# Optimization experiments

Hardware: AMD Instinct MI355X
Metric: run time of the kernel (lower is better)

The kernel has to match this reference:

```python
import jax, jax.numpy as jnp
import numpy as np

NUM_HEADS = 12

def setup_inputs() -> dict:
    key = jax.random.key(0)
    ks = jax.random.split(key, 6)
    B, N, C = 8, 1024, 768
    x = jax.random.normal(ks[0], (B, N, C), dtype=jnp.float32)
    qkv_w = jax.random.normal(ks[1], (3 * C, C), dtype=jnp.float32) * 0.02
    qkv_b = jax.random.normal(ks[2], (3 * C,), dtype=jnp.float32) * 0.02
    static_a = jax.random.normal(ks[3], (1, NUM_HEADS, N, N), dtype=jnp.float32) * 0.02
    proj_w = jax.random.normal(ks[4], (C, C), dtype=jnp.float32) * 0.02
    proj_b = jax.random.normal(ks[5], (C,), dtype=jnp.float32) * 0.02
    return {"x": x, "qkv_w": qkv_w, "qkv_b": qkv_b, "static_a": static_a,
            "proj_w": proj_w, "proj_b": proj_b}

def reference(x, qkv_w, qkv_b, static_a, proj_w, proj_b):
    B, N, C = x.shape
    H = NUM_HEADS
    D = C // H
    scale = D ** -0.5
    # qkv: [B,N,3C] -> [3,B,H,N,D]
    qkv = (x @ qkv_w.T + qkv_b).reshape(B, N, 3, H, D).transpose(2, 0, 3, 1, 4)
    q, k, v = qkv[0], qkv[1], qkv[2]
    attn = jnp.einsum('bhnd,bhmd->bhnm', q, k) * scale
    attn = jax.nn.softmax(attn, axis=-1)
    attn = attn + static_a  # static bias added AFTER softmax (no renorm)
    out = jnp.einsum('bhnm,bhmd->bhnd', attn, v)  # [B,H,N,D]
    out = out.transpose(0, 2, 1, 3).reshape(B, N, C)
    return out @ proj_w.T + proj_b
```

## Files before the change

kernel.cpp:

```cpp
#include <hip/hip_runtime.h>
#include <math.h>

#define NB   8
#define SEQ  1024
#define CH   768
#define NH   12
#define HD   64
#define BHT  (NB * NH)
#define QKVN 2304

typedef unsigned short u16;
typedef unsigned int   u32;
typedef __attribute__((ext_vector_type(8))) short bf16x8;
typedef __attribute__((ext_vector_type(4))) float f32x4;

__device__ __forceinline__ float bf2f(u32 s) {
    union { u32 u; float f; } v; v.u = s << 16; return v.f;
}
__device__ __forceinline__ u16 f2bf(float f) {
    union { float f; u32 u; } v; v.f = f;
    u32 u = v.u;
    return (u16)((u + 0x7fffu + ((u >> 16) & 1u)) >> 16);
}
__device__ __forceinline__ float ld1(const u16* p) { return bf2f((u32)*p); }
__device__ __forceinline__ void st1(u16* p, float v) { *p = f2bf(v); }
__device__ __forceinline__ void st1(float* p, float v) { *p = v; }
__device__ __forceinline__ void st4v(u16* p, float a, float b, float c, float d) {
    ushort4 o; o.x = f2bf(a); o.y = f2bf(b); o.z = f2bf(c); o.w = f2bf(d);
    *(ushort4*)p = o;
}
__device__ __forceinline__ void st4v(float* p, float a, float b, float c, float d) {
    float4 o; o.x = a; o.y = b; o.z = c; o.w = d;
    *(float4*)p = o;
}
__device__ __forceinline__ void gload16(const u16* g, u16* l) {
    __builtin_amdgcn_global_load_lds(
        (const __attribute__((address_space(1))) void*)g,
        (__attribute__((address_space(3))) void*)l, 16, 0, 0);
}

__global__ void detect_kernel(const u32* __restrict__ x, int* __restrict__ flag) {
    __shared__ int cnt;
    if (threadIdx.x == 0) cnt = 0;
    __syncthreads();
    int c = 0;
    for (int i = threadIdx.x; i < 2048; i += 256) {
        const u32 e0 = (x[i] >> 7) & 0xFFu;
        c += (e0 >= 110u && e0 <= 132u) ? 1 : 0;
    }
    atomicAdd(&cnt, c);
    __syncthreads();
    if (threadIdx.x == 0) *flag = (cnt > 1024) ? 1 : 0;
}

#define PREP_V4 5309184
__device__ __forceinline__ void prep_seg(size_t v, const size_t e0[6],
                                         int* segp, size_t* offp) {
    int seg = 5;
    if      (v < 1572864) seg = 0;
    else if (v < 2015232) seg = 1;
    else if (v < 2015808) seg = 2;
    else if (v < 5161536) seg = 3;
    else if (v < 5308992) seg = 4;
    *segp = seg; *offp = v * 4 - e0[seg];
}

__global__ __launch_bounds__(256) void prep_f32(
    const int* __restrict__ flag,
    const float* __restrict__ s0, const float* __restrict__ s1, const float* __restrict__ s2,
    const float* __restrict__ s3, const float* __restrict__ s4, const float* __restrict__ s5,
    u16* __restrict__ dst)
{
    if (*flag != 0) return;
    const float* const srcs[6] = {s0, s1, s2, s3, s4, s5};
    const size_t e0[6] = {0, 6291456, 8060928, 8063232, 20646144, 21235968};
    for (size_t v = blockIdx.x * 256 + threadIdx.x; v < PREP_V4; v += (size_t)gridDim.x * 256) {
        int seg; size_t off;
        prep_seg(v, e0, &seg, &off);
        const float4 f = *(const float4*)(srcs[seg] + off);
        ushort4 o; o.x = f2bf(f.x); o.y = f2bf(f.y); o.z = f2bf(f.z); o.w = f2bf(f.w);
        *(ushort4*)(dst + v * 4) = o;
    }
}

__global__ __launch_bounds__(256) void prep_bf16(
    const int* __restrict__ flag,
    const u16* __restrict__ s0, const u16* __restrict__ s1, const u16* __restrict__ s2,
    const u16* __restrict__ s3, const u16* __restrict__ s4, const u16* __restrict__ s5,
    u16* __restrict__ dst)
{
    if (*flag != 1) return;
    const u16* const srcs[6] = {s0, s1, s2, s3, s4, s5};
    const size_t e0[6] = {0, 6291456, 8060928, 8063232, 20646144, 21235968};
    for (size_t v = blockIdx.x * 256 + threadIdx.x; v < PREP_V4; v += (size_t)gridDim.x * 256) {
        int seg; size_t off;
        prep_seg(v, e0, &seg, &off);
        *(ushort4*)(dst + v * 4) = *(const ushort4*)(srcs[seg] + off);
    }
}

template<bool SWAP>
__device__ __forceinline__ void gemm128_core(
    const u16* __restrict__ Ag, const u16* __restrict__ Bg,
    f32x4 acc[4][4], u16* As, u16* Bs, int wm, int wn, int l15, int quad)
{
    const int t = threadIdx.x;
    const int w = t >> 6, lane = t & 63;
    const int lr = lane >> 2, lc = lane & 3;
    const int r0 = w * 16 + lr;
    const int r1 = 64 + w * 16 + lr;
    const int g0 = (lc + r0) & 3, g1 = (lc + r1) & 3;
    const u16* a0 = Ag + (size_t)r0 * CH + g0 * 8;
    const u16* a1 = Ag + (size_t)r1 * CH + g1 * 8;
    const u16* b0 = Bg + (size_t)r0 * CH + g0 * 8;
    const u16* b1 = Bg + (size_t)r1 * CH + g1 * 8;
    u16* lA0 = As + w * 512;
    u16* lA1 = As + 2048 + w * 512;
    u16* lB0 = Bs + w * 512;
    u16* lB1 = Bs + 2048 + w * 512;

#pragma unroll
    for (int mi = 0; mi < 4; mi++)
#pragma unroll
        for (int ni = 0; ni < 4; ni++) { f32x4 z = {0.f,0.f,0.f,0.f}; acc[mi][ni] = z; }

    for (int k0 = 0; k0 < CH; k0 += 32) {
        __syncthreads();
        gload16(a0 + k0, lA0);
        gload16(a1 + k0, lA1);
        gload16(b0 + k0, lB0);
        gload16(b1 + k0, lB1);
        __syncthreads();
        bf16x8 af[4], bfr[4];
#pragma unroll
        for (int mi = 0; mi < 4; mi++) {
            const int ra = wm * 64 + mi * 16 + l15;
            af[mi] = *(const bf16x8*)&As[ra * 32 + ((quad - ra) & 3) * 8];
        }
#pragma unroll
        for (int ni = 0; ni < 4; ni++) {
            const int rb = wn * 64 + ni * 16 + l15;
            bfr[ni] = *(const bf16x8*)&Bs[rb * 32 + ((quad - rb) & 3) * 8];
        }
#pragma unroll
        for (int mi = 0; mi < 4; mi++)
#pragma unroll
            for (int ni = 0; ni < 4; ni++)
                acc[mi][ni] = SWAP
                    ? __builtin_amdgcn_mfma_f32_16x16x32_bf16(bfr[ni], af[mi], acc[mi][ni], 0, 0, 0)
                    : __builtin_amdgcn_mfma_f32_16x16x32_bf16(af[mi], bfr[ni], acc[mi][ni], 0, 0, 0);
    }
}

__global__ __launch_bounds__(256) void qkv_gemm(
    const u16* __restrict__ x, const u16* __restrict__ w, const u16* __restrict__ bias,
    u16* __restrict__ Qn, u16* __restrict__ Kn, u16* __restrict__ Vt)
{
    __shared__ u16 As[128 * 32];
    __shared__ u16 Bs[128 * 32];
    const int t = threadIdx.x, lane = t & 63, wv = t >> 6;
    const int l15 = lane & 15, quad = lane >> 4;
    const int wm = wv >> 1, wn = wv & 1;
    const int m0 = blockIdx.y * 128, n0 = blockIdx.x * 128;
    const int which = n0 / CH;
    const int h     = ((n0 % CH) >> 6) + wn;
    const int b     = m0 >> 10;
    const size_t bh = (size_t)b * NH + h;
    const int sq0   = m0 & 1023;
    f32x4 acc[4][4];

    if (which == 2) {
        gemm128_core<false>(x + (size_t)m0 * CH, w + (size_t)n0 * CH,
                            acc, As, Bs, wm, wn, l15, quad);
        float bv[4];
#pragma unroll
        for (int ni = 0; ni < 4; ni++) bv[ni] = ld1(bias + n0 + wn * 64 + ni * 16 + l15);
#pragma unroll
        for (int mi = 0; mi < 4; mi++) {
            const int seq = sq0 + wm * 64 + mi * 16 + quad * 4;
#pragma unroll
            for (int ni = 0; ni < 4; ni++) {
                const int d = ni * 16 + l15;
                st4v(&Vt[(bh * HD + d) * SEQ + seq],
                     acc[mi][ni][0] + bv[ni], acc[mi][ni][1] + bv[ni],
                     acc[mi][ni][2] + bv[ni], acc[mi][ni][3] + bv[ni]);
            }
        }
    } else {
        gemm128_core<true>(x + (size_t)m0 * CH, w + (size_t)n0 * CH,
                           acc, As, Bs, wm, wn, l15, quad);
        u16* T2 = which ? Kn : Qn;
        const float qsc = which ? 1.0f : 0.125f;
        float bvr[4][4];
#pragma unroll
        for (int ni = 0; ni < 4; ni++)
#pragma unroll
            for (int r = 0; r < 4; r++)
                bvr[ni][r] = ld1(bias + n0 + wn * 64 + ni * 16 + quad * 4 + r);
#pragma unroll
        for (int mi = 0; mi < 4; mi++) {
            const int seq = sq0 + wm * 64 + mi * 16 + l15;
#pragma unroll
            for (int ni = 0; ni < 4; ni++) {
                const int dbase = ni * 16 + quad * 4;
                st4v(&T2[(bh * SEQ + seq) * HD + dbase],
                     (acc[mi][ni][0] + bvr[ni][0]) * qsc,
                     (acc[mi][ni][1] + bvr[ni][1]) * qsc,
                     (acc[mi][ni][2] + bvr[ni][2]) * qsc,
                     (acc[mi][ni][3] + bvr[ni][3]) * qsc);
            }
        }
    }
}

__global__ __launch_bounds__(256) void attn_kernel(
    const u16* __restrict__ Qn, const u16* __restrict__ Kn, const u16* __restrict__ Vt,
    const u16* __restrict__ Ab, u16* __restrict__ AO)
{
    __shared__ u16 Ks[64 * 72];
    __shared__ u16 Vs[64 * 72];
    __shared__ u16 Ps[4 * 32 * 72];

    const int qb = blockIdx.x;
    const int y  = blockIdx.y;
    const int hh = y >> 3, b = y & 7;
    const size_t bh = (size_t)b * NH + hh;
    const int t  = threadIdx.x;
    const int w  = t >> 6, lane = t & 63;
    const int l15 = lane & 15, quad = lane >> 4;
    const int sr = t >> 2, sc = (t & 3) * 16;
    const int i0g = qb * 128 + w * 32;
    u16* Psw = Ps + w * 32 * 72;

    bf16x8 qa[2][2];
#pragma unroll
    for (int isub = 0; isub < 2; isub++)
#pragma unroll
        for (int db = 0; db < 2; db++)
            qa[isub][db] = *(const bf16x8*)(Qn +
                (bh * SEQ + i0g + isub * 16 + l15) * HD + db * 32 + quad * 8);

    f32x4 Op[2][4], Oa[2][4];
#pragma unroll
    for (int i = 0; i < 2; i++)
#pragma unroll
        for (int d = 0; d < 4; d++) { f32x4 z = {0.f,0.f,0.f,0.f}; Op[i][d] = z; Oa[i][d] = z; }
    float rl[2][4] = {{0.f,0.f,0.f,0.f},{0.f,0.f,0.f,0.f}};

    for (int kt = 0; kt < 16; kt++) {
        const int j0 = kt * 64;
        bf16x8 afr[2][2];
#pragma unroll
        for (int jb = 0; jb < 2; jb++)
#pragma unroll
            for (int isub = 0; isub < 2; isub++)
                afr[jb][isub] = *(const bf16x8*)(Ab +
                    ((size_t)hh * SEQ + i0g + isub * 16 + l15) * SEQ
                    + j0 + jb * 32 + quad * 8);

        const u16* kp = Kn + (bh * SEQ + j0 + sr) * HD + sc;
        const u16* vp = Vt + (bh * HD + sr) * SEQ + j0 + sc;
        const uint4 k0v = *(const uint4*)kp, k1v = *(const uint4*)(kp + 8);
        const uint4 v0v = *(const uint4*)vp, v1v = *(const uint4*)(vp + 8);
        __syncthreads();
        *(uint4*)&Ks[sr * 72 + sc] = k0v; *(uint4*)&Ks[sr * 72 + sc + 8] = k1v;
        *(uint4*)&Vs[sr * 72 + sc] = v0v; *(uint4*)&Vs[sr * 72 + sc + 8] = v1v;
        __syncthreads();

#pragma unroll
        for (int j16 = 0; j16 < 4; j16++) {
            const bf16x8 kf0 = *(const bf16x8*)&Ks[(j16 * 16 + l15) * 72 + quad * 8];
            const bf16x8 kf1 = *(const bf16x8*)&Ks[(j16 * 16 + l15) * 72 + 32 + quad * 8];
#pragma unroll
            for (int isub = 0; isub < 2; isub++) {
                f32x4 s = {0.f, 0.f, 0.f, 0.f};
                s = __builtin_amdgcn_mfma_f32_16x16x32_bf16(qa[isub][0], kf0, s, 0, 0, 0);
                s = __builtin_amdgcn_mfma_f32_16x16x32_bf16(qa[isub][1], kf1, s, 0, 0, 0);
#pragma unroll
                for (int r = 0; r < 4; r++) {
                    const float p = __expf(fminf(s[r], 60.f));
                    rl[isub][r] += p;
                    Psw[(isub * 16 + quad * 4 + r) * 72 + j16 * 16 + l15] = f2bf(p);
                }
            }
        }

#pragma unroll
        for (int jb = 0; jb < 2; jb++) {
            bf16x8 pf[2];
#pragma unroll
            for (int isub = 0; isub < 2; isub++)
                pf[isub] = *(const bf16x8*)&Psw[(isub * 16 + l15) * 72 + jb * 32 + quad * 8];
#pragma unroll
            for (int d16 = 0; d16 < 4; d16++) {
                const bf16x8 vf = *(const bf16x8*)&Vs[(d16 * 16 + l15) * 72 + jb * 32 + quad * 8];
#pragma unroll
                for (int isub = 0; isub < 2; isub++) {
                    Op[isub][d16] = __builtin_amdgcn_mfma_f32_16x16x32_bf16(vf, pf[isub], Op[isub][d16], 0, 0, 0);
                    Oa[isub][d16] = __builtin_amdgcn_mfma_f32_16x16x32_bf16(vf, afr[jb][isub], Oa[isub][d16], 0, 0, 0);
                }
            }
        }
    }

    float inv[2];
#pragma unroll
    for (int isub = 0; isub < 2; isub++) {
        float rr[4];
#pragma unroll
        for (int r = 0; r < 4; r++) {
            float v = rl[isub][r];
            v += __shfl_xor(v, 1); v += __shfl_xor(v, 2);
            v += __shfl_xor(v, 4); v += __shfl_xor(v, 8);
            rr[r] = v;
        }
        const int src = (l15 >> 2) << 4;
        const float t0 = __shfl(rr[0], src), t1 = __shfl(rr[1], src);
        const float t2 = __shfl(rr[2], src), t3 = __shfl(rr[3], src);
        const float sel = (l15 & 2) ? ((l15 & 1) ? t3 : t2)
                                    : ((l15 & 1) ? t1 : t0);
        inv[isub] = 1.f / sel;
    }
#pragma unroll
    for (int isub = 0; isub < 2; isub++) {
        const int n = i0g + isub * 16 + l15;
#pragma unroll
        for (int d16 = 0; d16 < 4; d16++)
            st4v(&AO[((size_t)b * SEQ + n) * CH + hh * HD + d16 * 16 + quad * 4],
                 Op[isub][d16][0] * inv[isub] + Oa[isub][d16][0],
                 Op[isub][d16][1] * inv[isub] + Oa[isub][d16][1],
                 Op[isub][d16][2] * inv[isub] + Oa[isub][d16][2],
                 Op[isub][d16][3] * inv[isub] + Oa[isub][d16][3]);
    }
}

template<typename TO>
__global__ __launch_bounds__(256) void proj_gemm(
    const int* __restrict__ flag, const int want,
    const u16* __restrict__ AO, const u16* __restrict__ w, const u16* __restrict__ bias,
    TO* __restrict__ out)
{
    if (*flag != want) return;
    __shared__ u16 As[128 * 32];
    __shared__ u16 Bs[128 * 32];
    const int t = threadIdx.x, lane = t & 63, wv = t >> 6;
    const int l15 = lane & 15, quad = lane >> 4;
    const int wm = wv >> 1, wn = wv & 1;
    const int m0 = blockIdx.y * 128, n0 = blockIdx.x * 128;

    f32x4 acc[4][4];
    gemm128_core<true>(AO + (size_t)m0 * CH, w + (size_t)n0 * CH,
                       acc, As, Bs, wm, wn, l15, quad);

    float bvr[4][4];
#pragma unroll
    for (int ni = 0; ni < 4; ni++)
#pragma unroll
        for (int r = 0; r < 4; r++)
            bvr[ni][r] = ld1(bias + n0 + wn * 64 + ni * 16 + quad * 4 + r);
#pragma unroll
    for (int mi = 0; mi < 4; mi++) {
        const int m = m0 + wm * 64 + mi * 16 + l15;
#pragma unroll
        for (int ni = 0; ni < 4; ni++) {
            const int n = n0 + wn * 64 + ni * 16 + quad * 4;
            st4v(out + (size_t)m * CH + n,
                 acc[mi][ni][0] + bvr[ni][0], acc[mi][ni][1] + bvr[ni][1],
                 acc[mi][ni][2] + bvr[ni][2], acc[mi][ni][3] + bvr[ni][3]);
        }
    }
}

extern "C" void kernel_launch(void* const* d_in, const int* in_sizes, int n_in,
                              void* d_out, int out_size, void* d_ws, size_t ws_size,
                              hipStream_t stream) {
    (void)in_sizes; (void)n_in; (void)out_size; (void)ws_size;
    u16* ws = (u16*)d_ws;
    u16* xb   = ws;
    u16* wqb  = ws + 6291456;
    u16* bqb  = ws + 8060928;
    u16* Ab   = ws + 8063232;
    u16* pwb  = ws + 20646144;
    u16* pbb  = ws + 21235968;
    u16* arena_end = ws + 21236736;
    const size_t S1 = (size_t)NB * NH * SEQ * HD;
    u16* Qn = arena_end;
    u16* Kn = Qn + S1;
    u16* Vt = Kn + S1;
    u16* AO = Vt + S1;
    int* flag = (int*)(AO + S1);

    detect_kernel<<<dim3(1), dim3(256), 0, stream>>>((const u32*)d_in[0], flag);

    const dim3 blk(256);
    prep_f32 <<<dim3(4096), blk, 0, stream>>>(flag,
        (const float*)d_in[0], (const float*)d_in[1], (const float*)d_in[2],
        (const float*)d_in[3], (const float*)d_in[4], (const float*)d_in[5], ws);
    prep_bf16<<<dim3(4096), blk, 0, stream>>>(flag,
        (const u16*)d_in[0], (const u16*)d_in[1], (const u16*)d_in[2],
        (const u16*)d_in[3], (const u16*)d_in[4], (const u16*)d_in[5], ws);

    qkv_gemm<<<dim3(QKVN / 128, (NB * SEQ) / 128), blk, 0, stream>>>(
        xb, wqb, bqb, Qn, Kn, Vt);
    attn_kernel<<<dim3(SEQ / 128, BHT), blk, 0, stream>>>(Qn, Kn, Vt, Ab, AO);

    proj_gemm<float><<<dim3(CH / 128, (NB * SEQ) / 128), blk, 0, stream>>>(
        flag, 0, AO, pwb, pbb, (float*)d_out);
    proj_gemm<u16><<<dim3(CH / 128, (NB * SEQ) / 128), blk, 0, stream>>>(
        flag, 1, AO, pwb, pbb, (u16*)d_out);
}
```

Before: 276.6 us.

## Merge dtype-branch kernels and restructure attention to read K/V directly from global

The two dtype-specific prep kernels and the two projection GEMMs are each merged into one kernel that branches on the flag at runtime, removing two no-op launches. The attention kernel stops staging K and V through shared memory and loads MFMA fragments straight from global memory, which removes the block-level barriers. The QK^T MFMA operands are swapped so each lane holds a contiguous row of P, allowing packed bf16 conversion with v_cvt_pk_bf16_f32 and a simpler row-sum reduction. P is double-buffered per wave in LDS, and the kernel adds s_setprio hints and an occupancy hint of 3 blocks. The risk is that uncoalesced, duplicated global loads of K and V may cost more than the shared-memory staging did.

```diff
diff --git a/kernel.cpp b/kernel.cpp
--- a/kernel.cpp
+++ b/kernel.cpp
@@ -22,9 +22,12 @@
     u32 u = v.u;
     return (u16)((u + 0x7fffu + ((u >> 16) & 1u)) >> 16);
 }
+__device__ __forceinline__ u32 cvtpk(float lo, float hi) {
+    u32 r;
+    asm("v_cvt_pk_bf16_f32 %0, %1, %2" : "=v"(r) : "v"(lo), "v"(hi));
+    return r;
+}
 __device__ __forceinline__ float ld1(const u16* p) { return bf2f((u32)*p); }
-__device__ __forceinline__ void st1(u16* p, float v) { *p = f2bf(v); }
-__device__ __forceinline__ void st1(float* p, float v) { *p = v; }
 __device__ __forceinline__ void st4v(u16* p, float a, float b, float c, float d) {
     ushort4 o; o.x = f2bf(a); o.y = f2bf(b); o.z = f2bf(c); o.w = f2bf(d);
     *(ushort4*)p = o;
@@ -65,37 +68,31 @@
     *segp = seg; *offp = v * 4 - e0[seg];
 }
 
-__global__ __launch_bounds__(256) void prep_f32(
+__global__ __launch_bounds__(256) void prep_all(
     const int* __restrict__ flag,
-    const float* __restrict__ s0, const float* __restrict__ s1, const float* __restrict__ s2,
-    const float* __restrict__ s3, const float* __restrict__ s4, const float* __restrict__ s5,
+    const void* __restrict__ s0, const void* __restrict__ s1, const void* __restrict__ s2,
+    const void* __restrict__ s3, const void* __restrict__ s4, const void* __restrict__ s5,
     u16* __restrict__ dst)
 {
-    if (*flag != 0) return;
-    const float* const srcs[6] = {s0, s1, s2, s3, s4, s5};
     const size_t e0[6] = {0, 6291456, 8060928, 8063232, 20646144, 21235968};
-    for (size_t v = blockIdx.x * 256 + threadIdx.x; v < PREP_V4; v += (size_t)gridDim.x * 256) {
-        int seg; size_t off;
-        prep_seg(v, e0, &seg, &off);
-        const float4 f = *(const float4*)(srcs[seg] + off);
-        ushort4 o; o.x = f2bf(f.x); o.y = f2bf(f.y); o.z = f2bf(f.z); o.w = f2bf(f.w);
-        *(ushort4*)(dst + v * 4) = o;
-    }
-}
-
-__global__ __launch_bounds__(256) void prep_bf16(
-    const int* __restrict__ flag,
-    const u16* __restrict__ s0, const u16* __restrict__ s1, const u16* __restrict__ s2,
-    const u16* __restrict__ s3, const u16* __restrict__ s4, const u16* __restrict__ s5,
-    u16* __restrict__ dst)
-{
-    if (*flag != 1) return;
-    const u16* const srcs[6] = {s0, s1, s2, s3, s4, s5};
-    const size_t e0[6] = {0, 6291456, 8060928, 8063232, 20646144, 21235968};
-    for (size_t v = blockIdx.x * 256 + threadIdx.x; v < PREP_V4; v += (size_t)gridDim.x * 256) {
-        int seg; size_t off;
-        prep_seg(v, e0, &seg, &off);
-        *(ushort4*)(dst + v * 4) = *(const ushort4*)(srcs[seg] + off);
+    if (*flag != 0) {
+        const u16* const srcs[6] = {(const u16*)s0, (const u16*)s1, (const u16*)s2,
+                                    (const u16*)s3, (const u16*)s4, (const u16*)s5};
+        for (size_t v = blockIdx.x * 256 + threadIdx.x; v < PREP_V4; v += (size_t)gridDim.x * 256) {
+            int seg; size_t off;
+            prep_seg(v, e0, &seg, &off);
+            *(ushort4*)(dst + v * 4) = *(const ushort4*)(srcs[seg] + off);
+        }
+    } else {
+        const float* const srcs[6] = {(const float*)s0, (const float*)s1, (const float*)s2,
+                                      (const float*)s3, (const float*)s4, (const float*)s5};
+        for (size_t v = blockIdx.x * 256 + threadIdx.x; v < PREP_V4; v += (size_t)gridDim.x * 256) {
+            int seg; size_t off;
+            prep_seg(v, e0, &seg, &off);
+            const float4 f = *(const float4*)(srcs[seg] + off);
+            ushort4 o; o.x = f2bf(f.x); o.y = f2bf(f.y); o.z = f2bf(f.z); o.w = f2bf(f.w);
+            *(ushort4*)(dst + v * 4) = o;
+        }
     }
 }
 
@@ -213,13 +210,11 @@
     }
 }
 
-__global__ __launch_bounds__(256) void attn_kernel(
+__global__ __launch_bounds__(256, 3) void attn_kernel(
     const u16* __restrict__ Qn, const u16* __restrict__ Kn, const u16* __restrict__ Vt,
     const u16* __restrict__ Ab, u16* __restrict__ AO)
 {
-    __shared__ u16 Ks[64 * 72];
-    __shared__ u16 Vs[64 * 72];
-    __shared__ u16 Ps[4 * 32 * 72];
+    __shared__ u16 Ps[8 * 32 * 72];
 
     const int qb = blockIdx.x;
     const int y  = blockIdx.y;
@@ -228,9 +223,11 @@
     const int t  = threadIdx.x;
     const int w  = t >> 6, lane = t & 63;
     const int l15 = lane & 15, quad = lane >> 4;
-    const int sr = t >> 2, sc = (t & 3) * 16;
     const int i0g = qb * 128 + w * 32;
-    u16* Psw = Ps + w * 32 * 72;
+
+    const u16* Kb  = Kn + bh * SEQ * HD;
+    const u16* Vb  = Vt + bh * HD * SEQ;
+    const u16* Abr = Ab + (size_t)hh * SEQ * SEQ;
 
     bf16x8 qa[2][2];
 #pragma unroll
@@ -245,81 +242,67 @@
     for (int i = 0; i < 2; i++)
 #pragma unroll
         for (int d = 0; d < 4; d++) { f32x4 z = {0.f,0.f,0.f,0.f}; Op[i][d] = z; Oa[i][d] = z; }
-    float rl[2][4] = {{0.f,0.f,0.f,0.f},{0.f,0.f,0.f,0.f}};
+    float rl[2] = {0.f, 0.f};
 
     for (int kt = 0; kt < 16; kt++) {
         const int j0 = kt * 64;
+        u16* Psw = Ps + (w * 2 + (kt & 1)) * (32 * 72);
+
         bf16x8 afr[2][2];
 #pragma unroll
         for (int jb = 0; jb < 2; jb++)
 #pragma unroll
             for (int isub = 0; isub < 2; isub++)
-                afr[jb][isub] = *(const bf16x8*)(Ab +
-                    ((size_t)hh * SEQ + i0g + isub * 16 + l15) * SEQ
-                    + j0 + jb * 32 + quad * 8);
-
-        const u16* kp = Kn + (bh * SEQ + j0 + sr) * HD + sc;
-        const u16* vp = Vt + (bh * HD + sr) * SEQ + j0 + sc;
-        const uint4 k0v = *(const uint4*)kp, k1v = *(const uint4*)(kp + 8);
-        const uint4 v0v = *(const uint4*)vp, v1v = *(const uint4*)(vp + 8);
-        __syncthreads();
-        *(uint4*)&Ks[sr * 72 + sc] = k0v; *(uint4*)&Ks[sr * 72 + sc + 8] = k1v;
-        *(uint4*)&Vs[sr * 72 + sc] = v0v; *(uint4*)&Vs[sr * 72 + sc + 8] = v1v;
-        __syncthreads();
+                afr[jb][isub] = *(const bf16x8*)(Abr +
+                    (size_t)(i0g + isub * 16 + l15) * SEQ + j0 + jb * 32 + quad * 8);
 
 #pragma unroll
         for (int j16 = 0; j16 < 4; j16++) {
-            const bf16x8 kf0 = *(const bf16x8*)&Ks[(j16 * 16 + l15) * 72 + quad * 8];
-            const bf16x8 kf1 = *(const bf16x8*)&Ks[(j16 * 16 + l15) * 72 + 32 + quad * 8];
+            const u16* kr = Kb + (size_t)(j0 + j16 * 16 + l15) * HD + quad * 8;
+            const bf16x8 kf0 = *(const bf16x8*)kr;
+            const bf16x8 kf1 = *(const bf16x8*)(kr + 32);
 #pragma unroll
             for (int isub = 0; isub < 2; isub++) {
                 f32x4 s = {0.f, 0.f, 0.f, 0.f};
-                s = __builtin_amdgcn_mfma_f32_16x16x32_bf16(qa[isub][0], kf0, s, 0, 0, 0);
-                s = __builtin_amdgcn_mfma_f32_16x16x32_bf16(qa[isub][1], kf1, s, 0, 0, 0);
-#pragma unroll
-                for (int r = 0; r < 4; r++) {
-                    const float p = __expf(fminf(s[r], 60.f));
-                    rl[isub][r] += p;
-                    Psw[(isub * 16 + quad * 4 + r) * 72 + j16 * 16 + l15] = f2bf(p);
-                }
+                __builtin_amdgcn_s_setprio(1);
+                s = __builtin_amdgcn_mfma_f32_16x16x32_bf16(kf0, qa[isub][0], s, 0, 0, 0);
+                s = __builtin_amdgcn_mfma_f32_16x16x32_bf16(kf1, qa[isub][1], s, 0, 0, 0);
+                __builtin_amdgcn_s_setprio(0);
+                const float p0 = __expf(fminf(s[0], 60.f));
+                const float p1 = __expf(fminf(s[1], 60.f));
+                const float p2 = __expf(fminf(s[2], 60.f));
+                const float p3 = __expf(fminf(s[3], 60.f));
+                rl[isub] += (p0 + p1) + (p2 + p3);
+                uint2 u; u.x = cvtpk(p0, p1); u.y = cvtpk(p2, p3);
+                *(uint2*)&Psw[(isub * 16 + l15) * 72 + j16 * 16 + quad * 4] = u;
             }
         }
 
 #pragma unroll
         for (int jb = 0; jb < 2; jb++) {
-            bf16x8 pf[2];
-#pragma unroll
-            for (int isub = 0; isub < 2; isub++)
-                pf[isub] = *(const bf16x8*)&Psw[(isub * 16 + l15) * 72 + jb * 32 + quad * 8];
+            const bf16x8 pf0 = *(const bf16x8*)&Psw[(l15) * 72 + jb * 32 + quad * 8];
+            const bf16x8 pf1 = *(const bf16x8*)&Psw[(16 + l15) * 72 + jb * 32 + quad * 8];
+            __builtin_amdgcn_s_setprio(1);
 #pragma unroll
             for (int d16 = 0; d16 < 4; d16++) {
-                const bf16x8 vf = *(const bf16x8*)&Vs[(d16 * 16 + l15) * 72 + jb * 32 + quad * 8];
-#pragma unroll
-                for (int isub = 0; isub < 2; isub++) {
-                    Op[isub][d16] = __builtin_amdgcn_mfma_f32_16x16x32_bf16(vf, pf[isub], Op[isub][d16], 0, 0, 0);
-                    Oa[isub][d16] = __builtin_amdgcn_mfma_f32_16x16x32_bf16(vf, afr[jb][isub], Oa[isub][d16], 0, 0, 0);
-                }
+                const bf16x8 vf = *(const bf16x8*)(Vb +
+                    (size_t)(d16 * 16 + l15) * SEQ + j0 + jb * 32 + quad * 8);
+                Op[0][d16] = __builtin_amdgcn_mfma_f32_16x16x32_bf16(vf, pf0, Op[0][d16], 0, 0, 0);
+                Oa[0][d16] = __builtin_amdgcn_mfma_f32_16x16x32_bf16(vf, afr[jb][0], Oa[0][d16], 0, 0, 0);
+                Op[1][d16] = __builtin_amdgcn_mfma_f32_16x16x32_bf16(vf, pf1, Op[1][d16], 0, 0, 0);
+                Oa[1][d16] = __builtin_amdgcn_mfma_f32_16x16x32_bf16(vf, afr[jb][1], Oa[1][d16], 0, 0, 0);
             }
+            __builtin_amdgcn_s_setprio(0);
         }
     }
 
     float inv[2];
 #pragma unroll
     for (int isub = 0; isub < 2; isub++) {
-        float rr[4];
-#pragma unroll
-        for (int r = 0; r < 4; r++) {
-            float v = rl[isub][r];
-            v += __shfl_xor(v, 1); v += __shfl_xor(v, 2);
-            v += __shfl_xor(v, 4); v += __shfl_xor(v, 8);
-            rr[r] = v;
-        }
-        const int src = (l15 >> 2) << 4;
-        const float t0 = __shfl(rr[0], src), t1 = __shfl(rr[1], src);
-        const float t2 = __shfl(rr[2], src), t3 = __shfl(rr[3], src);
-        const float sel = (l15 & 2) ? ((l15 & 1) ? t3 : t2)
-                                    : ((l15 & 1) ? t1 : t0);
-        inv[isub] = 1.f / sel;
+        float v = rl[isub];
+        v += __shfl_xor(v, 16);
+        v += __shfl_xor(v, 32);
+        inv[isub] = 1.f / v;
     }
 #pragma unroll
     for (int isub = 0; isub < 2; isub++) {
@@ -334,15 +317,14 @@
     }
 }
 
-template<typename TO>
-__global__ __launch_bounds__(256) void proj_gemm(
-    const int* __restrict__ flag, const int want,
+__global__ __launch_bounds__(256) void proj_all(
+    const int* __restrict__ flag,
     const u16* __restrict__ AO, const u16* __restrict__ w, const u16* __restrict__ bias,
-    TO* __restrict__ out)
-{
-    if (*flag != want) return;
+    void* __restrict__ outv)
+{
     __shared__ u16 As[128 * 32];
     __shared__ u16 Bs[128 * 32];
+    const int isbf = *flag;
     const int t = threadIdx.x, lane = t & 63, wv = t >> 6;
     const int l15 = lane & 15, quad = lane >> 4;
     const int wm = wv >> 1, wn = wv & 1;
@@ -364,9 +346,14 @@
 #pragma unroll
         for (int ni = 0; ni < 4; ni++) {
             const int n = n0 + wn * 64 + ni * 16 + quad * 4;
-            st4v(out + (size_t)m * CH + n,
-                 acc[mi][ni][0] + bvr[ni][0], acc[mi][ni][1] + bvr[ni][1],
-                 acc[mi][ni][2] + bvr[ni][2], acc[mi][ni][3] + bvr[ni][3]);
+            if (isbf)
+                st4v((u16*)outv + (size_t)m * CH + n,
+                     acc[mi][ni][0] + bvr[ni][0], acc[mi][ni][1] + bvr[ni][1],
+                     acc[mi][ni][2] + bvr[ni][2], acc[mi][ni][3] + bvr[ni][3]);
+            else
+                st4v((float*)outv + (size_t)m * CH + n,
+                     acc[mi][ni][0] + bvr[ni][0], acc[mi][ni][1] + bvr[ni][1],
+                     acc[mi][ni][2] + bvr[ni][2], acc[mi][ni][3] + bvr[ni][3]);
         }
     }
 }
@@ -393,19 +380,13 @@
     detect_kernel<<<dim3(1), dim3(256), 0, stream>>>((const u32*)d_in[0], flag);
 
     const dim3 blk(256);
-    prep_f32 <<<dim3(4096), blk, 0, stream>>>(flag,
-        (const float*)d_in[0], (const float*)d_in[1], (const float*)d_in[2],
-        (const float*)d_in[3], (const float*)d_in[4], (const float*)d_in[5], ws);
-    prep_bf16<<<dim3(4096), blk, 0, stream>>>(flag,
-        (const u16*)d_in[0], (const u16*)d_in[1], (const u16*)d_in[2],
-        (const u16*)d_in[3], (const u16*)d_in[4], (const u16*)d_in[5], ws);
+    prep_all<<<dim3(4096), blk, 0, stream>>>(flag,
+        d_in[0], d_in[1], d_in[2], d_in[3], d_in[4], d_in[5], ws);
 
     qkv_gemm<<<dim3(QKVN / 128, (NB * SEQ) / 128), blk, 0, stream>>>(
         xb, wqb, bqb, Qn, Kn, Vt);
     attn_kernel<<<dim3(SEQ / 128, BHT), blk, 0, stream>>>(Qn, Kn, Vt, Ab, AO);
 
-    proj_gemm<float><<<dim3(CH / 128, (NB * SEQ) / 128), blk, 0, stream>>>(
-        flag, 0, AO, pwb, pbb, (float*)d_out);
-    proj_gemm<u16><<<dim3(CH / 128, (NB * SEQ) / 128), blk, 0, stream>>>(
-        flag, 1, AO, pwb, pbb, (u16*)d_out);
-}
+    proj_all<<<dim3(CH / 128, (NB * SEQ) / 128), blk, 0, stream>>>(
+        flag, AO, pwb, pbb, d_out);
+}
```

After: 326.1 us. 1.18x slower.
